# Kernel tuning notes

Hardware: AMD Instinct MI355X
Metric: run time of the kernel (lower is better)

## Reference

```python
import jax, jax.numpy as jnp
import numpy as np

SIGMA = 1.0
SQRT2 = float(np.sqrt(2.0))


def setup_inputs() -> dict:
    key = jax.random.key(0)
    k1, k2 = jax.random.split(key)
    B, L = 128, 1024
    preds = jax.random.normal(k1, (B, L), dtype=jnp.float32)
    # integer relevance grades 0..4, stored as float as in the torch module
    target = jax.random.randint(k2, (B, L), 0, 5).astype(jnp.float32)
    return {"preds": preds, "target": target}


def reference(preds, target):
    B, L = preds.shape
    # pairwise diff [B, L, L]: diff[b,i,j] = preds[b,i] - preds[b,j]
    diff = preds[:, :, None] - preds[:, None, :]
    # Normal(0, sigma*sqrt(2)).cdf(diff) == ndtr(diff / (sigma*sqrt(2)))
    p = jax.scipy.special.ndtr(diff / (SIGMA * SQRT2))
    # zero the diagonal (i == j) before summing
    eye = jnp.eye(L, dtype=bool)
    p = jnp.where(eye[None, :, :], 0.0, p)
    expected_ranks = 1.0 + p.sum(axis=2)  # [B, L]

    gains = 2.0 ** target - 1.0
    discounts = jnp.log2(expected_ranks + 1.0)
    dcg = (gains / discounts).sum(axis=1)  # [B]

    ideal_target = jnp.sort(target, axis=1)[:, ::-1]  # descending
    ideal_gains = 2.0 ** ideal_target - 1.0
    ideal_discounts = jnp.log2(jnp.arange(1, L + 1, dtype=jnp.float32) + 1.0)
    idcg = (ideal_gains / ideal_discounts).sum(axis=1)  # [B]

    ndcg = dcg / (idcg + 1e-10)
    return -ndcg.mean()
```

## Files before the change

kernel.cpp:

```cpp
#include <hip/hip_runtime.h>
#include <hip/hip_fp16.h>

#define B 128
#define L 1024
#define NTILE 24
#define TSTRIDE 576

#if __has_builtin(__builtin_amdgcn_exp2f)
#define EXP2(x) __builtin_amdgcn_exp2f(x)
#else
#define EXP2(x) __expf((x) * 0.6931471805599453f)
#endif

typedef unsigned int uint4v __attribute__((ext_vector_type(4)));

#define WS_ACC  (B * NTILE * TSTRIDE)
#define WS_GCTR (WS_ACC + 1)

#define K1f -1.6279072f
#define K2f -0.9299637f
#define K3f -0.1074808f

__device__ __forceinline__ __half2 term2v(unsigned int du, __half2 pi2,
                                          __half2 k1, __half2 k2, __half2 k3,
                                          __half2 one2) {
    __half2 pj = __builtin_bit_cast(__half2, du);
    __half2 d  = __hsub2(pi2, pj);
    unsigned int dbits = __builtin_bit_cast(unsigned int, d);
    __half2 a  = __builtin_bit_cast(__half2, dbits & 0x7fff7fffu);
    __half2 t  = __hfma2(k3, a, k2);
    __half2 u  = __hfma2(t,  a, k1);
    __half2 w  = __hmul2(a, u);
    __half2 e  = __halves2half2(hexp2(__low2half(w)),
                                hexp2(__high2half(w)));
    __half2 r  = __hsub2(one2, e);
    unsigned int rs = (dbits & 0x80008000u)
                    | (__builtin_bit_cast(unsigned int, r) & 0x7fff7fffu);
    return __builtin_bit_cast(__half2, rs);
}

__global__ __launch_bounds__(256, 8) void pair_kernel(const float* __restrict__ preds,
                                                      const float* __restrict__ target,
                                                      float* __restrict__ ws) {
    __shared__ __align__(16) unsigned char smem[2048 + 8192 + 8192];
    __half* sph = (__half*)smem;
    float* rowLDS = (float*)(smem + 2048);
    unsigned int* colLDS = (unsigned int*)(smem + 2048 + 8192);
    float* col2LDS = (float*)smem;

    const int blk = blockIdx.x;
    const int b   = blk / NTILE;
    const int tl  = blk - b * NTILE;
    const int r   = (tl >= 16) ? 1 : 0;
    const int q   = r ? (tl - 8) : tl;
    const int tid = threadIdx.x;
    const int il  = tid & 63;
    const int jq  = tid >> 6;

    if (blk == 0 && tid == 0) {
        ws[WS_ACC] = 0.0f;
        ((int*)ws)[WS_GCTR] = 0;
    }

    const float* prow = preds + b * L;
    float4 v4 = reinterpret_cast<const float4*>(prow)[tid];
    reinterpret_cast<__half2*>(sph)[tid * 2 + 0] = __floats2half2_rn(0.5f * v4.x, 0.5f * v4.y);
    reinterpret_cast<__half2*>(sph)[tid * 2 + 1] = __floats2half2_rn(0.5f * v4.z, 0.5f * v4.w);
    __syncthreads();

    const __half2 k1   = __floats2half2_rn(K1f, K1f);
    const __half2 k2   = __floats2half2_rn(K2f, K2f);
    const __half2 k3   = __floats2half2_rn(K3f, K3f);
    const __half2 one2 = __floats2half2_rn(1.0f, 1.0f);
    const __half2 z2   = __floats2half2_rn(0.0f, 0.0f);

    const uint4v* cp4 = reinterpret_cast<const uint4v*>(sph + q * 64 + jq * 16);
    uint4v pq0 = cp4[0], pq1 = cp4[1];
    unsigned int pjb[8] = {pq0.x, pq0.y, pq0.z, pq0.w, pq1.x, pq1.y, pq1.z, pq1.w};

    __half2 colacc[8] = {z2, z2, z2, z2, z2, z2, z2, z2};

    const int r8 = r << 3;
    for (int rr = 0; rr < 8; ++rr) {
        const int s = r8 + rr;
        if (s > q) break;
        const bool ca = (s < q);
        const __half2 pi2 = __half2half2(sph[(s << 6) + il]);
        __half2 A = z2, Bc = z2;
        #pragma unroll
        for (int m = 0; m < 8; ++m) {
            __half2 tm = term2v(pjb[m], pi2, k1, k2, k3, one2);
            if (m < 4) A = __hadd2(A, tm); else Bc = __hadd2(Bc, tm);
            if (ca) colacc[m] = __hadd2(colacc[m], tm);
        }
        float2 fA = __half22float2(A), fB = __half22float2(Bc);
        rowLDS[(rr << 8) + (jq << 6) + il] = (fA.x + fA.y) + (fB.x + fB.y);
    }

    #pragma unroll
    for (int m = 0; m < 8; ++m)
        colLDS[((jq << 3) + m) * 64 + il] = __builtin_bit_cast(unsigned int, colacc[m]);
    __syncthreads();

    float* wst = ws + (b * NTILE + tl) * TSTRIDE;

    #pragma unroll
    for (int h = 0; h < 2; ++h) {
        int rho = tid + (h << 8);
        int rrx = rho >> 6, ilx = rho & 63;
        float v = (rowLDS[(rrx << 8) + ilx]       + rowLDS[(rrx << 8) + 64 + ilx])
                + (rowLDS[(rrx << 8) + 128 + ilx] + rowLDS[(rrx << 8) + 192 + ilx]);
        wst[rho] = v;
    }

    {
        int cp = tid & 31, ilq = tid >> 5;
        const uint4v* cl = reinterpret_cast<const uint4v*>(colLDS + cp * 64 + ilq * 8);
        uint4v c0 = cl[0], c1 = cl[1];
        unsigned int cc[8] = {c0.x, c0.y, c0.z, c0.w, c1.x, c1.y, c1.z, c1.w};
        float sx = 0.0f, sy = 0.0f;
        #pragma unroll
        for (int k = 0; k < 8; ++k) {
            float2 f = __half22float2(__builtin_bit_cast(__half2, cc[k]));
            sx += f.x; sy += f.y;
        }
        col2LDS[ilq * 64 + cp * 2 + 0] = sx;
        col2LDS[ilq * 64 + cp * 2 + 1] = sy;
    }
    __syncthreads();

    if (tid < 64) {
        float cs = 0.0f;
        #pragma unroll
        for (int g = 0; g < 8; ++g) cs += col2LDS[g * 64 + tid];
        wst[512 + tid] = cs;
    }
}

__global__ __launch_bounds__(256) void finish_kernel(const float* __restrict__ target,
                                                     float* __restrict__ ws,
                                                     float* __restrict__ out) {
    __shared__ unsigned long long cred[256];
    __shared__ float2 fred[256];

    const int b   = blockIdx.x;
    const int tid = threadIdx.x;
    const float* trow = target + b * L;

    float tv[4];
    unsigned long long cnt = 0ull;
    #pragma unroll
    for (int k = 0; k < 4; ++k) {
        float t = trow[tid + k * 256];
        tv[k] = t;
        cnt += ((unsigned long long)(t > 3.5f) << 48)
             + ((unsigned long long)(t > 2.5f) << 32)
             + ((unsigned long long)(t > 1.5f) << 16)
             + ((unsigned long long)(t > 0.5f));
    }
    cred[tid] = cnt;
    __syncthreads();
    #pragma unroll
    for (int s = 128; s > 0; s >>= 1) {
        if (tid < (unsigned)s) cred[tid] += cred[tid + s];
        __syncthreads();
    }
    unsigned long long tot = cred[0];
    const int n4 = (int)(tot >> 48) & 0xFFFF;
    const int n3 = (int)(tot >> 32) & 0xFFFF;
    const int n2 = (int)(tot >> 16) & 0xFFFF;
    const int n1 = (int)(tot)       & 0xFFFF;

    float idcg_p = 0.0f;
    #pragma unroll
    for (int k = 0; k < 4; ++k) {
        int pos = tid + 1 + k * 256;
        float gain = (pos <= n4) ? 15.0f : (pos <= n3) ? 7.0f :
                     (pos <= n2) ? 3.0f  : (pos <= n1) ? 1.0f : 0.0f;
        idcg_p += gain * __builtin_amdgcn_rcpf(__log2f((float)pos + 1.0f));
    }

    const int b24 = b * NTILE;
    float dcg_p = 0.0f;
    #pragma unroll
    for (int k = 0; k < 4; ++k) {
        int i  = tid + (k << 8);
        int u  = i >> 6;
        int rb = u >> 3;
        int rho = i & 511;
        float rowsum = 0.0f;
        for (int qq = u; qq < 16; ++qq)
            rowsum += ws[(b24 + qq + (rb << 3)) * TSTRIDE + rho];
        float cols = 0.0f;
        int i6 = i & 63;
        if (u >= 1) cols += ws[(b24 + u) * TSTRIDE + 512 + i6];
        if (u >= 9) cols += ws[(b24 + u + 8) * TSTRIDE + 512 + i6];
        float Es  = rowsum - cols;
        float er1 = 513.5f + 0.5f * Es;
        float g   = EXP2(tv[k]) - 1.0f;
        dcg_p += g * __builtin_amdgcn_rcpf(__log2f(er1));
    }

    fred[tid] = make_float2(idcg_p, dcg_p);
    __syncthreads();
    #pragma unroll
    for (int s = 128; s > 0; s >>= 1) {
        if (tid < (unsigned)s) {
            float2 x = fred[tid], y = fred[tid + s];
            fred[tid] = make_float2(x.x + y.x, x.y + y.y);
        }
        __syncthreads();
    }

    if (tid == 0) {
        float ndcg = fred[0].y / (fred[0].x + 1e-10f);
        atomicAdd(&ws[WS_ACC], ndcg);
        __threadfence();
        int old = atomicAdd((int*)ws + WS_GCTR, 1);
        if (old == B - 1) {
            float acc = atomicAdd(&ws[WS_ACC], 0.0f);
            out[0] = -acc * (1.0f / (float)B);
        }
    }
}

extern "C" void kernel_launch(void* const* d_in, const int* in_sizes, int n_in,
                              void* d_out, int out_size, void* d_ws, size_t ws_size,
                              hipStream_t stream) {
    const float* preds  = (const float*)d_in[0];
    const float* target = (const float*)d_in[1];
    float* out = (float*)d_out;
    float* ws  = (float*)d_ws;

    pair_kernel<<<B * NTILE, 256, 0, stream>>>(preds, target, ws);
    finish_kernel<<<B, 256, 0, stream>>>(target, ws, out);
}
```

Baseline: 95.44 us.

## Pair tiles for load balance and split row gather into separate kernel

The pair kernel now launches 16 blocks per batch row instead of 24. Blocks 0-7 each process two tiles (kk and 23-kk), pairing triangular tiles of different sizes to even out work per block. The per-row gather of partial sums, previously done serially in 128 finish blocks, moves into a new 512-block gather kernel that writes per-element DCG terms to workspace, and the finish kernel only sums them. This adds a kernel launch, an extra workspace round trip, and more barriers inside the tile loop.

New measurement: 89.00 us. -6.7%, faster.

```diff
diff --git a/kernel.cpp b/kernel.cpp
--- a/kernel.cpp
+++ b/kernel.cpp
@@ -14,7 +14,8 @@
 
 typedef unsigned int uint4v __attribute__((ext_vector_type(4)));
 
-#define WS_ACC  (B * NTILE * TSTRIDE)
+#define WS2     (B * NTILE * TSTRIDE)
+#define WS_ACC  (WS2 + B * L)
 #define WS_GCTR (WS_ACC + 1)
 
 #define K1f -1.6279072f
@@ -46,13 +47,11 @@
     __half* sph = (__half*)smem;
     float* rowLDS = (float*)(smem + 2048);
     unsigned int* colLDS = (unsigned int*)(smem + 2048 + 8192);
-    float* col2LDS = (float*)smem;
+    float* col2LDS = (float*)(smem + 2048 + 8192);
 
     const int blk = blockIdx.x;
-    const int b   = blk / NTILE;
-    const int tl  = blk - b * NTILE;
-    const int r   = (tl >= 16) ? 1 : 0;
-    const int q   = r ? (tl - 8) : tl;
+    const int b   = blk >> 4;
+    const int kk  = blk & 15;
     const int tid = threadIdx.x;
     const int il  = tid & 63;
     const int jq  = tid >> 6;
@@ -74,67 +73,103 @@
     const __half2 one2 = __floats2half2_rn(1.0f, 1.0f);
     const __half2 z2   = __floats2half2_rn(0.0f, 0.0f);
 
-    const uint4v* cp4 = reinterpret_cast<const uint4v*>(sph + q * 64 + jq * 16);
-    uint4v pq0 = cp4[0], pq1 = cp4[1];
-    unsigned int pjb[8] = {pq0.x, pq0.y, pq0.z, pq0.w, pq1.x, pq1.y, pq1.z, pq1.w};
-
-    __half2 colacc[8] = {z2, z2, z2, z2, z2, z2, z2, z2};
-
-    const int r8 = r << 3;
-    for (int rr = 0; rr < 8; ++rr) {
-        const int s = r8 + rr;
-        if (s > q) break;
-        const bool ca = (s < q);
-        const __half2 pi2 = __half2half2(sph[(s << 6) + il]);
-        __half2 A = z2, Bc = z2;
+    const int ntl = (kk < 8) ? 2 : 1;
+    for (int tt = 0; tt < ntl; ++tt) {
+        const int tl = tt ? (23 - kk) : kk;
+        const int r  = (tl >= 16) ? 1 : 0;
+        const int q  = r ? (tl - 8) : tl;
+
+        const uint4v* cp4 = reinterpret_cast<const uint4v*>(sph + q * 64 + jq * 16);
+        uint4v pq0 = cp4[0], pq1 = cp4[1];
+        unsigned int pjb[8] = {pq0.x, pq0.y, pq0.z, pq0.w, pq1.x, pq1.y, pq1.z, pq1.w};
+
+        __half2 colacc[8] = {z2, z2, z2, z2, z2, z2, z2, z2};
+
+        const int r8 = r << 3;
+        for (int rr = 0; rr < 8; ++rr) {
+            const int s = r8 + rr;
+            if (s > q) break;
+            const bool ca = (s < q);
+            const __half2 pi2 = __half2half2(sph[(s << 6) + il]);
+            __half2 A = z2, Bc = z2;
+            #pragma unroll
+            for (int m = 0; m < 8; ++m) {
+                __half2 tm = term2v(pjb[m], pi2, k1, k2, k3, one2);
+                if (m < 4) A = __hadd2(A, tm); else Bc = __hadd2(Bc, tm);
+                if (ca) colacc[m] = __hadd2(colacc[m], tm);
+            }
+            float2 fA = __half22float2(A), fB = __half22float2(Bc);
+            rowLDS[(rr << 8) + (jq << 6) + il] = (fA.x + fA.y) + (fB.x + fB.y);
+        }
+
         #pragma unroll
-        for (int m = 0; m < 8; ++m) {
-            __half2 tm = term2v(pjb[m], pi2, k1, k2, k3, one2);
-            if (m < 4) A = __hadd2(A, tm); else Bc = __hadd2(Bc, tm);
-            if (ca) colacc[m] = __hadd2(colacc[m], tm);
-        }
-        float2 fA = __half22float2(A), fB = __half22float2(Bc);
-        rowLDS[(rr << 8) + (jq << 6) + il] = (fA.x + fA.y) + (fB.x + fB.y);
-    }
-
-    #pragma unroll
-    for (int m = 0; m < 8; ++m)
-        colLDS[((jq << 3) + m) * 64 + il] = __builtin_bit_cast(unsigned int, colacc[m]);
-    __syncthreads();
-
-    float* wst = ws + (b * NTILE + tl) * TSTRIDE;
-
-    #pragma unroll
-    for (int h = 0; h < 2; ++h) {
-        int rho = tid + (h << 8);
-        int rrx = rho >> 6, ilx = rho & 63;
-        float v = (rowLDS[(rrx << 8) + ilx]       + rowLDS[(rrx << 8) + 64 + ilx])
-                + (rowLDS[(rrx << 8) + 128 + ilx] + rowLDS[(rrx << 8) + 192 + ilx]);
-        wst[rho] = v;
-    }
-
-    {
-        int cp = tid & 31, ilq = tid >> 5;
-        const uint4v* cl = reinterpret_cast<const uint4v*>(colLDS + cp * 64 + ilq * 8);
-        uint4v c0 = cl[0], c1 = cl[1];
-        unsigned int cc[8] = {c0.x, c0.y, c0.z, c0.w, c1.x, c1.y, c1.z, c1.w};
+        for (int m = 0; m < 8; ++m)
+            colLDS[((jq << 3) + m) * 64 + il] = __builtin_bit_cast(unsigned int, colacc[m]);
+        __syncthreads();
+
+        float* wst = ws + (b * NTILE + tl) * TSTRIDE;
+
+        #pragma unroll
+        for (int h = 0; h < 2; ++h) {
+            int rho = tid + (h << 8);
+            int rrx = rho >> 6, ilx = rho & 63;
+            float v = (rowLDS[(rrx << 8) + ilx]       + rowLDS[(rrx << 8) + 64 + ilx])
+                    + (rowLDS[(rrx << 8) + 128 + ilx] + rowLDS[(rrx << 8) + 192 + ilx]);
+            wst[rho] = v;
+        }
+
         float sx = 0.0f, sy = 0.0f;
-        #pragma unroll
-        for (int k = 0; k < 8; ++k) {
-            float2 f = __half22float2(__builtin_bit_cast(__half2, cc[k]));
-            sx += f.x; sy += f.y;
-        }
-        col2LDS[ilq * 64 + cp * 2 + 0] = sx;
-        col2LDS[ilq * 64 + cp * 2 + 1] = sy;
-    }
-    __syncthreads();
-
-    if (tid < 64) {
-        float cs = 0.0f;
-        #pragma unroll
-        for (int g = 0; g < 8; ++g) cs += col2LDS[g * 64 + tid];
-        wst[512 + tid] = cs;
-    }
+        {
+            int cp = tid & 31, ilq = tid >> 5;
+            const uint4v* cl = reinterpret_cast<const uint4v*>(colLDS + cp * 64 + ilq * 8);
+            uint4v c0 = cl[0], c1 = cl[1];
+            unsigned int cc[8] = {c0.x, c0.y, c0.z, c0.w, c1.x, c1.y, c1.z, c1.w};
+            #pragma unroll
+            for (int m = 0; m < 8; ++m) {
+                float2 f = __half22float2(__builtin_bit_cast(__half2, cc[m]));
+                sx += f.x; sy += f.y;
+            }
+        }
+        __syncthreads();
+        {
+            int cp = tid & 31, ilq = tid >> 5;
+            col2LDS[ilq * 64 + cp * 2 + 0] = sx;
+            col2LDS[ilq * 64 + cp * 2 + 1] = sy;
+        }
+        __syncthreads();
+
+        if (tid < 64) {
+            float cs = 0.0f;
+            #pragma unroll
+            for (int g = 0; g < 8; ++g) cs += col2LDS[g * 64 + tid];
+            wst[512 + tid] = cs;
+        }
+        __syncthreads();
+    }
+}
+
+__global__ __launch_bounds__(256) void gather_kernel(const float* __restrict__ target,
+                                                     float* __restrict__ ws) {
+    const int blk = blockIdx.x;
+    const int b   = blk >> 2;
+    const int i   = ((blk & 3) << 8) + threadIdx.x;
+    const int u   = i >> 6;
+    const int rb  = u >> 3;
+    const int rho = i & 511;
+    const int i6  = i & 63;
+    const int b24 = b * NTILE;
+
+    float rowsum = 0.0f;
+    for (int qq = u; qq < 16; ++qq)
+        rowsum += ws[(b24 + qq + (rb << 3)) * TSTRIDE + rho];
+    float cols = 0.0f;
+    if (u >= 1) cols += ws[(b24 + u) * TSTRIDE + 512 + i6];
+    if (u >= 9) cols += ws[(b24 + u + 8) * TSTRIDE + 512 + i6];
+
+    float Es  = rowsum - cols;
+    float er1 = 513.5f + 0.5f * Es;
+    float g   = EXP2(target[b * L + i]) - 1.0f;
+    ws[WS2 + b * L + i] = g * __builtin_amdgcn_rcpf(__log2f(er1));
 }
 
 __global__ __launch_bounds__(256) void finish_kernel(const float* __restrict__ target,
@@ -147,12 +182,10 @@
     const int tid = threadIdx.x;
     const float* trow = target + b * L;
 
-    float tv[4];
     unsigned long long cnt = 0ull;
     #pragma unroll
     for (int k = 0; k < 4; ++k) {
         float t = trow[tid + k * 256];
-        tv[k] = t;
         cnt += ((unsigned long long)(t > 3.5f) << 48)
              + ((unsigned long long)(t > 2.5f) << 32)
              + ((unsigned long long)(t > 1.5f) << 16)
@@ -172,33 +205,14 @@
     const int n1 = (int)(tot)       & 0xFFFF;
 
     float idcg_p = 0.0f;
+    float dcg_p  = 0.0f;
     #pragma unroll
     for (int k = 0; k < 4; ++k) {
         int pos = tid + 1 + k * 256;
         float gain = (pos <= n4) ? 15.0f : (pos <= n3) ? 7.0f :
                      (pos <= n2) ? 3.0f  : (pos <= n1) ? 1.0f : 0.0f;
         idcg_p += gain * __builtin_amdgcn_rcpf(__log2f((float)pos + 1.0f));
-    }
-
-    const int b24 = b * NTILE;
-    float dcg_p = 0.0f;
-    #pragma unroll
-    for (int k = 0; k < 4; ++k) {
-        int i  = tid + (k << 8);
-        int u  = i >> 6;
-        int rb = u >> 3;
-        int rho = i & 511;
-        float rowsum = 0.0f;
-        for (int qq = u; qq < 16; ++qq)
-            rowsum += ws[(b24 + qq + (rb << 3)) * TSTRIDE + rho];
-        float cols = 0.0f;
-        int i6 = i & 63;
-        if (u >= 1) cols += ws[(b24 + u) * TSTRIDE + 512 + i6];
-        if (u >= 9) cols += ws[(b24 + u + 8) * TSTRIDE + 512 + i6];
-        float Es  = rowsum - cols;
-        float er1 = 513.5f + 0.5f * Es;
-        float g   = EXP2(tv[k]) - 1.0f;
-        dcg_p += g * __builtin_amdgcn_rcpf(__log2f(er1));
+        dcg_p  += ws[WS2 + b * L + tid + k * 256];
     }
 
     fred[tid] = make_float2(idcg_p, dcg_p);
@@ -232,6 +246,7 @@
     float* out = (float*)d_out;
     float* ws  = (float*)d_ws;
 
-    pair_kernel<<<B * NTILE, 256, 0, stream>>>(preds, target, ws);
+    pair_kernel<<<B * 16, 256, 0, stream>>>(preds, target, ws);
+    gather_kernel<<<B * 4, 256, 0, stream>>>(target, ws);
     finish_kernel<<<B, 256, 0, stream>>>(target, ws, out);
 }
```
